# Performance work log

Measured on AMD Instinct MI355X. Metric: run time of the kernel, lower is better.

The kernel has to match this reference:

```python
import jax, jax.numpy as jnp
import numpy as np

NUM_GRAPHS = 5 * 0 + 64  # number of graphs in the batch
NUM_CLASSES = 5


def gcn_conv(x, src, dst, W, b, n_nodes):
    """PyG GCNConv: x' = D^{-1/2} (A+I) D^{-1/2} x W + b (self-loops already in src/dst)."""
    h = x @ W  # [N, out]
    deg = jax.ops.segment_sum(jnp.ones(dst.shape, h.dtype), dst, num_segments=n_nodes)
    dinv = deg ** -0.5  # deg >= 1 thanks to self-loops
    norm = dinv[src] * dinv[dst]  # [E+N]
    msg = h[src] * norm[:, None]  # gather + normalize
    out = jax.ops.segment_sum(msg, dst, num_segments=n_nodes)  # scatter-add
    return out + b


def setup_inputs() -> dict:
    key = jax.random.key(0)
    ks = jax.random.split(key, 12)
    N, E, D_IN, D_H, D_F = 50000, 500000, 128, 256, 256
    x = jax.random.normal(ks[0], (N, D_IN), dtype=jnp.float32)
    edge_index = jax.random.randint(ks[1], (2, E), 0, N, dtype=jnp.int64)
    batch = jnp.sort(jax.random.randint(ks[2], (N,), 0, NUM_GRAPHS, dtype=jnp.int64))
    def lin(k, fi, fo):
        s = 1.0 / np.sqrt(fi)
        return jax.random.uniform(k, (fi, fo), jnp.float32, -s, s)
    return {
        "x": x, "edge_index": edge_index, "batch": batch,
        "W0": lin(ks[3], D_IN, D_H), "b0": jnp.zeros((D_H,), jnp.float32),
        "W1": lin(ks[4], D_H, D_H),  "b1": jnp.zeros((D_H,), jnp.float32),
        "W2": lin(ks[5], D_H, D_H),  "b2": jnp.zeros((D_H,), jnp.float32),
        "Wc1": lin(ks[6], D_H, D_F), "bc1": jnp.zeros((D_F,), jnp.float32),
        "Wc2": lin(ks[7], D_F, NUM_CLASSES), "bc2": jnp.zeros((NUM_CLASSES,), jnp.float32),
    }


def reference(x, edge_index, batch, W0, b0, W1, b1, W2, b2, Wc1, bc1, Wc2, bc2):
    n_nodes = x.shape[0]
    loops = jnp.arange(n_nodes, dtype=edge_index.dtype)
    src = jnp.concatenate([edge_index[0], loops])
    dst = jnp.concatenate([edge_index[1], loops])

    h = jax.nn.relu(gcn_conv(x, src, dst, W0, b0, n_nodes))
    h = jax.nn.relu(gcn_conv(h, src, dst, W1, b1, n_nodes))
    h = jax.nn.relu(gcn_conv(h, src, dst, W2, b2, n_nodes))

    # global_mean_pool over batch ids
    sums = jax.ops.segment_sum(h, batch, num_segments=NUM_GRAPHS)
    cnts = jax.ops.segment_sum(jnp.ones((n_nodes,), h.dtype), batch, num_segments=NUM_GRAPHS)
    g = sums / jnp.maximum(cnts, 1.0)[:, None]  # [NUM_GRAPHS, D_H]

    # classifier MLP (dropout inactive at eval)
    out = jax.nn.relu(g @ Wc1 + bc1) @ Wc2 + bc2
    return out
```

## Files before the change

### kernel.cpp

```cpp
#include <hip/hip_runtime.h>
#include <hip/hip_fp16.h>

typedef short s16x8 __attribute__((ext_vector_type(8)));
typedef float fx4 __attribute__((ext_vector_type(4)));

#define AS_G(p) ((const __attribute__((address_space(1))) void*)(p))
#define AS_L(p) ((__attribute__((address_space(3))) void*)(p))

struct __align__(8) half4 { __half2 lo, hi; };

__device__ inline unsigned short f32_to_bf16(float f) {
    unsigned int u = __float_as_uint(f);
    return (unsigned short)((u + 0x7fffu + ((u >> 16) & 1u)) >> 16);
}
__device__ inline float bf16_to_f32(unsigned short b) {
    return __uint_as_float(((unsigned int)b) << 16);
}
__device__ inline void split2(float a, unsigned short& hi, unsigned short& lo) {
    hi = f32_to_bf16(a);
    lo = f32_to_bf16(a - bf16_to_f32(hi));
}


__global__ void k_degx(const int* __restrict__ dst, int E, int* __restrict__ deg, int degB,
                       const float* __restrict__ x, __half* __restrict__ xh, int nx) {
    if (blockIdx.x < (unsigned)degB) {
        int i = blockIdx.x * 256 + threadIdx.x;
        if (i < E) atomicAdd(&deg[dst[i]], 1);
    } else {
        int i = (blockIdx.x - degB) * 1024 + threadIdx.x * 4;
        if (i < nx) {
            float4 v = *(const float4*)&x[i];
            __half2 h0(__float2half(v.x), __float2half(v.y));
            __half2 h1(__float2half(v.z), __float2half(v.w));
            *(__half2*)&xh[i] = h0;
            *(__half2*)&xh[i + 2] = h1;
        }
    }
}

__global__ void k_scan1w(const int* __restrict__ deg, int N, int nb,
                         int* __restrict__ part, int* __restrict__ bsum, float* __restrict__ dinv,
                         const float* __restrict__ W0, unsigned short* __restrict__ h0, unsigned short* __restrict__ l0,
                         const float* __restrict__ W1, unsigned short* __restrict__ h1, unsigned short* __restrict__ l1,
                         const float* __restrict__ W2, unsigned short* __restrict__ h2, unsigned short* __restrict__ l2,
                         int DIN, int DH) {
    __shared__ int s[256];
    if (blockIdx.x < (unsigned)nb) {
        int i = blockIdx.x * 256 + threadIdx.x;
        int v = (i < N) ? deg[i] : 0;
        if (i < N) dinv[i] = 1.0f / sqrtf((float)(v + 1));
        s[threadIdx.x] = v;
        __syncthreads();
        for (int off = 1; off < 256; off <<= 1) {
            int t = (threadIdx.x >= off) ? s[threadIdx.x - off] : 0;
            __syncthreads();
            s[threadIdx.x] += t;
            __syncthreads();
        }
        if (i < N) part[i] = s[threadIdx.x] - v;
        if (threadIdx.x == 255) bsum[blockIdx.x] = s[255];
    } else {
        int i = (blockIdx.x - nb) * 256 + threadIdx.x;
        const int n0 = DIN * DH, n1 = DH * DH;
        const float* W; unsigned short *hT, *lT; int K, li;
        if (i < n0) { W = W0; hT = h0; lT = l0; K = DIN; li = i; }
        else if (i < n0 + n1) { W = W1; hT = h1; lT = l1; K = DH; li = i - n0; }
        else if (i < n0 + 2 * n1) { W = W2; hT = h2; lT = l2; K = DH; li = i - n0 - n1; }
        else return;
        int k = li / DH, n = li - k * DH;
        unsigned short h, l;
        split2(W[li], h, l);
        hT[(size_t)n * K + k] = h;
        lT[(size_t)n * K + k] = l;
    }
}

__global__ void k_scan2(int* __restrict__ bsum, int nb,
                        const int* __restrict__ batch, int N, int ngraphs, int* __restrict__ gstart) {
    int g = threadIdx.x;
    if (g <= ngraphs) {
        if (g == ngraphs) gstart[g] = N;
        else {
            int lo = 0, hi = N;
            while (lo < hi) {
                int mid = (lo + hi) >> 1;
                if (batch[mid] < g) lo = mid + 1; else hi = mid;
            }
            gstart[g] = lo;
        }
    }
    __shared__ int s[256];
    int v = (threadIdx.x < nb) ? bsum[threadIdx.x] : 0;
    s[threadIdx.x] = v;
    __syncthreads();
    for (int off = 1; off < 256; off <<= 1) {
        int t = (threadIdx.x >= off) ? s[threadIdx.x - off] : 0;
        __syncthreads();
        s[threadIdx.x] += t;
        __syncthreads();
    }
    if (threadIdx.x < nb) bsum[threadIdx.x] = s[threadIdx.x] - v;
}

__global__ void k_scan3(const int* __restrict__ part, const int* __restrict__ bsum, int N, int E,
                        int* __restrict__ rowptr, int* __restrict__ cursor) {
    int i = blockIdx.x * 256 + threadIdx.x;
    if (i < N) {
        int v = part[i] + bsum[blockIdx.x];
        rowptr[i] = v;
        cursor[i] = v;
    }
    if (i == 0) rowptr[N] = E;
}

__global__ void k_fill(const int* __restrict__ src, const int* __restrict__ dst, int E,
                       const float* __restrict__ dinv, int* __restrict__ cursor,
                       int* __restrict__ col, float* __restrict__ nrm) {
    int e = blockIdx.x * blockDim.x + threadIdx.x;
    if (e < E) {
        int s = src[e], d = dst[e];
        int p = atomicAdd(&cursor[d], 1);
        col[p] = s;
        nrm[p] = dinv[s] * dinv[d];
    }
}


__global__ __launch_bounds__(256) void k_gemm_mfma(
    const unsigned short* __restrict__ Ahi, const unsigned short* __restrict__ Alo,
    const unsigned short* __restrict__ BhiT, const unsigned short* __restrict__ BloT,
    const float* __restrict__ bias, __half* __restrict__ C, int Nrows, int K) {
    __shared__ __align__(16) unsigned short sAhi[128 * 32];
    __shared__ __align__(16) unsigned short sAlo[128 * 32];
    __shared__ __align__(16) unsigned short sBhi[128 * 32];
    __shared__ __align__(16) unsigned short sBlo[128 * 32];

    const int tid = threadIdx.x;
    const int wid = tid >> 6, lane = tid & 63;
    const int row0 = blockIdx.y * 128;
    const int col0 = blockIdx.x * 128;
    const int wrow = wid & 1, wcol = wid >> 1;
    const int quad = lane >> 4, l16 = lane & 15;

    const unsigned short* garr = (wid == 0) ? Ahi : (wid == 1) ? Alo : (wid == 2) ? BhiT : BloT;
    unsigned short* sarr = (wid == 0) ? sAhi : (wid == 1) ? sAlo : (wid == 2) ? sBhi : sBlo;
    const bool isA = (wid < 2);

    const unsigned short* gp[8];
#pragma unroll
    for (int i = 0; i < 8; ++i) {
        int r = 16 * i + (lane >> 2);
        int s = lane & 3;
        int q = (s - (r >> 1)) & 3;
        int grow = isA ? min(row0 + r, Nrows - 1) : (col0 + r);
        gp[i] = garr + (size_t)grow * K + q * 8;
    }

    int aidx[4], bidx[4];
#pragma unroll
    for (int t = 0; t < 4; ++t) {
        int ra = wrow * 64 + t * 16 + l16;
        aidx[t] = ra * 32 + ((quad + (ra >> 1)) & 3) * 8;
        int rb = wcol * 64 + t * 16 + l16;
        bidx[t] = rb * 32 + ((quad + (rb >> 1)) & 3) * 8;
    }

    fx4 acc[4][4] = {};

    for (int k0 = 0; k0 < K; k0 += 32) {
#pragma unroll
        for (int i = 0; i < 8; ++i)
            __builtin_amdgcn_global_load_lds(AS_G(gp[i] + k0), AS_L((char*)sarr + i * 1024), 16, 0, 0);
        __syncthreads();

        s16x8 ah[4], al[4];
#pragma unroll
        for (int mi = 0; mi < 4; ++mi) {
            ah[mi] = *(const s16x8*)&sAhi[aidx[mi]];
            al[mi] = *(const s16x8*)&sAlo[aidx[mi]];
        }
#pragma unroll
        for (int nj = 0; nj < 4; ++nj) {
            s16x8 bh = *(const s16x8*)&sBhi[bidx[nj]];
            s16x8 bl = *(const s16x8*)&sBlo[bidx[nj]];
#pragma unroll
            for (int mi = 0; mi < 4; ++mi) {
                acc[mi][nj] = __builtin_amdgcn_mfma_f32_16x16x32_bf16(ah[mi], bh, acc[mi][nj], 0, 0, 0);
                acc[mi][nj] = __builtin_amdgcn_mfma_f32_16x16x32_bf16(ah[mi], bl, acc[mi][nj], 0, 0, 0);
                acc[mi][nj] = __builtin_amdgcn_mfma_f32_16x16x32_bf16(al[mi], bh, acc[mi][nj], 0, 0, 0);
            }
        }
        __syncthreads();
    }

#pragma unroll
    for (int mi = 0; mi < 4; ++mi) {
        const int rbase = row0 + wrow * 64 + mi * 16 + quad * 4;
#pragma unroll
        for (int nj = 0; nj < 4; ++nj) {
            const int c = col0 + wcol * 64 + nj * 16 + l16;
            const float bc = bias[c];
#pragma unroll
            for (int reg = 0; reg < 4; ++reg) {
                int r = rbase + reg;
                if (r < Nrows) C[(size_t)r * 256 + c] = __float2half(fmaxf(acc[mi][nj][reg] + bc, 0.f));
            }
        }
    }
}

__global__ __launch_bounds__(256) void k_gemm_pool(
    const unsigned short* __restrict__ Ahi, const unsigned short* __restrict__ Alo,
    const unsigned short* __restrict__ BhiT, const unsigned short* __restrict__ BloT,
    const float* __restrict__ bias, const int* __restrict__ batch,
    float* __restrict__ gsum, int Nrows, int K) {
    __shared__ __align__(16) unsigned short sAhi[128 * 32];
    __shared__ __align__(16) unsigned short sAlo[128 * 32];
    __shared__ __align__(16) unsigned short sBhi[128 * 32];
    __shared__ __align__(16) unsigned short sBlo[128 * 32];

    const int tid = threadIdx.x;
    const int wid = tid >> 6, lane = tid & 63;
    const int row0 = blockIdx.y * 128;
    const int col0 = blockIdx.x * 128;
    const int wrow = wid & 1, wcol = wid >> 1;
    const int quad = lane >> 4, l16 = lane & 15;

    const unsigned short* garr = (wid == 0) ? Ahi : (wid == 1) ? Alo : (wid == 2) ? BhiT : BloT;
    unsigned short* sarr = (wid == 0) ? sAhi : (wid == 1) ? sAlo : (wid == 2) ? sBhi : sBlo;
    const bool isA = (wid < 2);

    const unsigned short* gp[8];
#pragma unroll
    for (int i = 0; i < 8; ++i) {
        int r = 16 * i + (lane >> 2);
        int s = lane & 3;
        int q = (s - (r >> 1)) & 3;
        int grow = isA ? min(row0 + r, Nrows - 1) : (col0 + r);
        gp[i] = garr + (size_t)grow * K + q * 8;
    }

    int aidx[4], bidx[4];
#pragma unroll
    for (int t = 0; t < 4; ++t) {
        int ra = wrow * 64 + t * 16 + l16;
        aidx[t] = ra * 32 + ((quad + (ra >> 1)) & 3) * 8;
        int rb = wcol * 64 + t * 16 + l16;
        bidx[t] = rb * 32 + ((quad + (rb >> 1)) & 3) * 8;
    }

    fx4 acc[4][4] = {};

    for (int k0 = 0; k0 < K; k0 += 32) {
#pragma unroll
        for (int i = 0; i < 8; ++i)
            __builtin_amdgcn_global_load_lds(AS_G(gp[i] + k0), AS_L((char*)sarr + i * 1024), 16, 0, 0);
        __syncthreads();

        s16x8 ah[4], al[4];
#pragma unroll
        for (int mi = 0; mi < 4; ++mi) {
            ah[mi] = *(const s16x8*)&sAhi[aidx[mi]];
            al[mi] = *(const s16x8*)&sAlo[aidx[mi]];
        }
#pragma unroll
        for (int nj = 0; nj < 4; ++nj) {
            s16x8 bh = *(const s16x8*)&sBhi[bidx[nj]];
            s16x8 bl = *(const s16x8*)&sBlo[bidx[nj]];
#pragma unroll
            for (int mi = 0; mi < 4; ++mi) {
                acc[mi][nj] = __builtin_amdgcn_mfma_f32_16x16x32_bf16(ah[mi], bh, acc[mi][nj], 0, 0, 0);
                acc[mi][nj] = __builtin_amdgcn_mfma_f32_16x16x32_bf16(ah[mi], bl, acc[mi][nj], 0, 0, 0);
                acc[mi][nj] = __builtin_amdgcn_mfma_f32_16x16x32_bf16(al[mi], bh, acc[mi][nj], 0, 0, 0);
            }
        }
        __syncthreads();
    }

    int bg[4][4];
#pragma unroll
    for (int mi = 0; mi < 4; ++mi)
#pragma unroll
        for (int reg = 0; reg < 4; ++reg) {
            int r = row0 + wrow * 64 + mi * 16 + quad * 4 + reg;
            bg[mi][reg] = (r < Nrows) ? batch[r] : -1;
        }
    const int gfirst = batch[row0 < Nrows ? row0 : (Nrows - 1)];
    const int glast  = batch[min(row0 + 127, Nrows - 1)];

#pragma unroll
    for (int nj = 0; nj < 4; ++nj) {
        const int c = col0 + wcol * 64 + nj * 16 + l16;
        const float bc = bias[c];
        for (int g = gfirst; g <= glast; ++g) {
            float s = 0.f;
#pragma unroll
            for (int mi = 0; mi < 4; ++mi)
#pragma unroll
                for (int reg = 0; reg < 4; ++reg)
                    if (bg[mi][reg] == g) s += fmaxf(acc[mi][nj][reg] + bc, 0.f);
            s += __shfl_xor(s, 16);
            s += __shfl_xor(s, 32);
            if (quad == 0) atomicAdd(&gsum[g * 256 + c], s);
        }
    }
}


__global__ __launch_bounds__(256) void k_agg256(const __half* __restrict__ H, const int* __restrict__ rowptr,
                                                const int* __restrict__ col, const float* __restrict__ nrm,
                                                const float* __restrict__ dinv,
                                                unsigned short* __restrict__ outHi,
                                                unsigned short* __restrict__ outLo, int N) {
    const int wave = threadIdx.x >> 6, lane = threadIdx.x & 63;
    const int v = blockIdx.x * 4 + wave;
    if (v >= N) return;

    const float di = dinv[v];
    const float selfn = di * di;
    half4 hv = ((const half4*)&H[(size_t)v * 256])[lane];
    float2 s0 = __half22float2(hv.lo), s1 = __half22float2(hv.hi);
    float ax = selfn * s0.x, ay = selfn * s0.y, az = selfn * s1.x, aw = selfn * s1.y;

    int e = rowptr[v];
    const int end = rowptr[v + 1];
    for (; e + 8 <= end; e += 8) {
        int u[8]; float w[8]; half4 g[8];
#pragma unroll
        for (int j = 0; j < 8; ++j) { u[j] = col[e + j]; w[j] = nrm[e + j]; }
#pragma unroll
        for (int j = 0; j < 8; ++j) g[j] = ((const half4*)&H[(size_t)u[j] * 256])[lane];
#pragma unroll
        for (int j = 0; j < 8; ++j) {
            float2 f0 = __half22float2(g[j].lo), f1 = __half22float2(g[j].hi);
            ax += w[j] * f0.x; ay += w[j] * f0.y; az += w[j] * f1.x; aw += w[j] * f1.y;
        }
    }
    for (; e < end; ++e) {
        const int u = col[e];
        const float w = nrm[e];
        half4 g = ((const half4*)&H[(size_t)u * 256])[lane];
        float2 f0 = __half22float2(g.lo), f1 = __half22float2(g.hi);
        ax += w * f0.x; ay += w * f0.y; az += w * f1.x; aw += w * f1.y;
    }

    ushort4 hi4, lo4;
    split2(ax, hi4.x, lo4.x);
    split2(ay, hi4.y, lo4.y);
    split2(az, hi4.z, lo4.z);
    split2(aw, hi4.w, lo4.w);
    ((ushort4*)outHi)[(size_t)v * 64 + lane] = hi4;
    ((ushort4*)outLo)[(size_t)v * 64 + lane] = lo4;
}

__global__ __launch_bounds__(256) void k_agg128(const __half* __restrict__ X, const int* __restrict__ rowptr,
                                                const int* __restrict__ col, const float* __restrict__ nrm,
                                                const float* __restrict__ dinv,
                                                unsigned short* __restrict__ outHi,
                                                unsigned short* __restrict__ outLo, int N) {
    const int half = threadIdx.x >> 5, sub = threadIdx.x & 31;
    const int v = blockIdx.x * 8 + half;
    if (v >= N) return;

    const float di = dinv[v];
    const float selfn = di * di;
    half4 hv = ((const half4*)&X[(size_t)v * 128])[sub];
    float2 s0 = __half22float2(hv.lo), s1 = __half22float2(hv.hi);
    float ax = selfn * s0.x, ay = selfn * s0.y, az = selfn * s1.x, aw = selfn * s1.y;

    int e = rowptr[v];
    const int end = rowptr[v + 1];
    for (; e + 4 <= end; e += 4) {
        int u[4]; float w[4]; half4 g[4];
#pragma unroll
        for (int j = 0; j < 4; ++j) { u[j] = col[e + j]; w[j] = nrm[e + j]; }
#pragma unroll
        for (int j = 0; j < 4; ++j) g[j] = ((const half4*)&X[(size_t)u[j] * 128])[sub];
#pragma unroll
        for (int j = 0; j < 4; ++j) {
            float2 f0 = __half22float2(g[j].lo), f1 = __half22float2(g[j].hi);
            ax += w[j] * f0.x; ay += w[j] * f0.y; az += w[j] * f1.x; aw += w[j] * f1.y;
        }
    }
    for (; e < end; ++e) {
        const int u = col[e];
        const float w = nrm[e];
        half4 g = ((const half4*)&X[(size_t)u * 128])[sub];
        float2 f0 = __half22float2(g.lo), f1 = __half22float2(g.hi);
        ax += w * f0.x; ay += w * f0.y; az += w * f1.x; aw += w * f1.y;
    }

    ushort4 hi4, lo4;
    split2(ax, hi4.x, lo4.x);
    split2(ay, hi4.y, lo4.y);
    split2(az, hi4.z, lo4.z);
    split2(aw, hi4.w, lo4.w);
    ((ushort4*)outHi)[(size_t)v * 32 + sub] = hi4;
    ((ushort4*)outLo)[(size_t)v * 32 + sub] = lo4;
}


__global__ __launch_bounds__(256) void k_poolcls(const float* __restrict__ gsum, const int* __restrict__ gstart,
                                                 const float* __restrict__ Wc1, const float* __restrict__ bc1,
                                                 const float* __restrict__ Wc2, const float* __restrict__ bc2,
                                                 float* __restrict__ out) {
    __shared__ float sg[256], sh[256];
    const int b = blockIdx.x, t = threadIdx.x;
    const float c = (float)(gstart[b + 1] - gstart[b]);
    sg[t] = gsum[b * 256 + t] / fmaxf(c, 1.0f);
    __syncthreads();
    float acc = bc1[t];
    for (int k = 0; k < 256; ++k) acc += sg[k] * Wc1[k * 256 + t];
    sh[t] = fmaxf(acc, 0.f);
    __syncthreads();
    if (t < 5) {
        float o = bc2[t];
        for (int k = 0; k < 256; ++k) o += sh[k] * Wc2[k * 5 + t];
        out[b * 5 + t] = o;
    }
}


extern "C" void kernel_launch(void* const* d_in, const int* in_sizes, int n_in,
                              void* d_out, int out_size, void* d_ws, size_t ws_size,
                              hipStream_t stream) {
    const float* x    = (const float*)d_in[0];
    const int*   eidx = (const int*)d_in[1];
    const int*   batch= (const int*)d_in[2];
    const float* W0 = (const float*)d_in[3];  const float* b0 = (const float*)d_in[4];
    const float* W1 = (const float*)d_in[5];  const float* b1 = (const float*)d_in[6];
    const float* W2 = (const float*)d_in[7];  const float* b2 = (const float*)d_in[8];
    const float* Wc1= (const float*)d_in[9];  const float* bc1= (const float*)d_in[10];
    const float* Wc2= (const float*)d_in[11]; const float* bc2= (const float*)d_in[12];
    float* out = (float*)d_out;

    const int N   = in_sizes[2];
    const int E   = in_sizes[1] / 2;
    const int DIN = in_sizes[0] / N;
    const int DH  = in_sizes[4];
    const int* src = eidx;
    const int* dst = eidx + E;

    char* p = (char*)d_ws;
    auto alloc = [&](size_t bytes) {
        char* r = p;
        p += (bytes + 255) & ~(size_t)255;
        return (void*)r;
    };
    __half*         hbuf = (__half*)alloc((size_t)N * DH * 2);
    __half*         xh   = (__half*)alloc((size_t)N * DIN * 2);
    unsigned short* hhi  = (unsigned short*)alloc((size_t)N * DH * 2);
    unsigned short* hlo  = (unsigned short*)alloc((size_t)N * DH * 2);
    unsigned short* w0hi = (unsigned short*)alloc((size_t)DH * DIN * 2);
    unsigned short* w0lo = (unsigned short*)alloc((size_t)DH * DIN * 2);
    unsigned short* w1hi = (unsigned short*)alloc((size_t)DH * DH * 2);
    unsigned short* w1lo = (unsigned short*)alloc((size_t)DH * DH * 2);
    unsigned short* w2hi = (unsigned short*)alloc((size_t)DH * DH * 2);
    unsigned short* w2lo = (unsigned short*)alloc((size_t)DH * DH * 2);
    int*   deg   = (int*)alloc((size_t)N * 4);
    float* gsum  = (float*)alloc(64 * (size_t)DH * 4);
    float* dinv  = (float*)alloc((size_t)N * 4);
    int*   part  = (int*)alloc((size_t)N * 4);
    int*   bsum  = (int*)alloc(256 * 4);
    int*   rowptr= (int*)alloc((size_t)(N + 1) * 4);
    int*   cursor= (int*)alloc((size_t)N * 4);
    int*   col   = (int*)alloc((size_t)E * 4);
    float* nrm   = (float*)alloc((size_t)E * 4);
    int*   gstart= (int*)alloc(65 * 4);

    hipMemsetAsync(deg, 0, (size_t)((char*)gsum - (char*)deg) + 64 * (size_t)DH * 4, stream);

    const int nb = (N + 255) / 256;
    const int wtot = DIN * DH + 2 * DH * DH;
    const int wb = (wtot + 255) / 256;
    const int degB = (E + 255) / 256;
    const int nx = N * DIN;
    const int xb = (nx + 1023) / 1024;

    k_degx  <<<degB + xb, 256, 0, stream>>>(dst, E, deg, degB, x, xh, nx);
    k_scan1w<<<nb + wb, 256, 0, stream>>>(deg, N, nb, part, bsum, dinv,
                                          W0, w0hi, w0lo, W1, w1hi, w1lo, W2, w2hi, w2lo, DIN, DH);
    k_scan2 <<<1, 256, 0, stream>>>(bsum, nb, batch, N, 64, gstart);
    k_scan3 <<<nb, 256, 0, stream>>>(part, bsum, N, E, rowptr, cursor);
    k_fill  <<<(E + 255) / 256, 256, 0, stream>>>(src, dst, E, dinv, cursor, col, nrm);

    dim3 gemmGrid(DH / 128, (N + 127) / 128);

    k_agg128<<<(N + 7) / 8, 256, 0, stream>>>(xh, rowptr, col, nrm, dinv, hhi, hlo, N);
    k_gemm_mfma<<<gemmGrid, 256, 0, stream>>>(hhi, hlo, w0hi, w0lo, b0, hbuf, N, DIN);
    k_agg256<<<(N + 3) / 4, 256, 0, stream>>>(hbuf, rowptr, col, nrm, dinv, hhi, hlo, N);
    k_gemm_mfma<<<gemmGrid, 256, 0, stream>>>(hhi, hlo, w1hi, w1lo, b1, hbuf, N, DH);
    k_agg256<<<(N + 3) / 4, 256, 0, stream>>>(hbuf, rowptr, col, nrm, dinv, hhi, hlo, N);
    k_gemm_pool<<<gemmGrid, 256, 0, stream>>>(hhi, hlo, w2hi, w2lo, b2, batch, gsum, N, DH);

    k_poolcls<<<64, 256, 0, stream>>>(gsum, gstart, Wc1, bc1, Wc2, bc2, out);
}
```

Before: 397.3 us.

## Double-buffer GEMM LDS tiles and fold scan2 into scan3 and poolcls

Both MFMA GEMM kernels now use two LDS buffers, issuing global-to-LDS loads for the next K chunk before computing the current one, with one barrier per iteration instead of two. The single-block k_scan2 launch is removed: each scan3 block reduces the preceding block sums itself, and the graph-boundary binary search moves into k_poolcls. This cuts a serialized launch and overlaps memory loads with MFMA work. In exchange LDS use doubles to 64KB per block, which may lower occupancy, and the async LDS writes into the other buffer may need a wait before the barrier to be correct.

```diff
diff --git a/kernel.cpp b/kernel.cpp
--- a/kernel.cpp
+++ b/kernel.cpp
@@ -76,38 +76,20 @@
     }
 }
 
-__global__ void k_scan2(int* __restrict__ bsum, int nb,
-                        const int* __restrict__ batch, int N, int ngraphs, int* __restrict__ gstart) {
-    int g = threadIdx.x;
-    if (g <= ngraphs) {
-        if (g == ngraphs) gstart[g] = N;
-        else {
-            int lo = 0, hi = N;
-            while (lo < hi) {
-                int mid = (lo + hi) >> 1;
-                if (batch[mid] < g) lo = mid + 1; else hi = mid;
-            }
-            gstart[g] = lo;
-        }
-    }
+__global__ void k_scan3(const int* __restrict__ part, const int* __restrict__ bsum, int nb,
+                        int N, int E, int* __restrict__ rowptr, int* __restrict__ cursor) {
     __shared__ int s[256];
-    int v = (threadIdx.x < nb) ? bsum[threadIdx.x] : 0;
-    s[threadIdx.x] = v;
+    const int t = threadIdx.x;
+    s[t] = (t < nb && t < (int)blockIdx.x) ? bsum[t] : 0;
     __syncthreads();
-    for (int off = 1; off < 256; off <<= 1) {
-        int t = (threadIdx.x >= off) ? s[threadIdx.x - off] : 0;
+    for (int off = 128; off > 0; off >>= 1) {
+        if (t < off) s[t] += s[t + off];
         __syncthreads();
-        s[threadIdx.x] += t;
-        __syncthreads();
-    }
-    if (threadIdx.x < nb) bsum[threadIdx.x] = s[threadIdx.x] - v;
-}
-
-__global__ void k_scan3(const int* __restrict__ part, const int* __restrict__ bsum, int N, int E,
-                        int* __restrict__ rowptr, int* __restrict__ cursor) {
-    int i = blockIdx.x * 256 + threadIdx.x;
+    }
+    const int base = s[0];
+    int i = blockIdx.x * 256 + t;
     if (i < N) {
-        int v = part[i] + bsum[blockIdx.x];
+        int v = part[i] + base;
         rowptr[i] = v;
         cursor[i] = v;
     }
@@ -131,10 +113,7 @@
     const unsigned short* __restrict__ Ahi, const unsigned short* __restrict__ Alo,
     const unsigned short* __restrict__ BhiT, const unsigned short* __restrict__ BloT,
     const float* __restrict__ bias, __half* __restrict__ C, int Nrows, int K) {
-    __shared__ __align__(16) unsigned short sAhi[128 * 32];
-    __shared__ __align__(16) unsigned short sAlo[128 * 32];
-    __shared__ __align__(16) unsigned short sBhi[128 * 32];
-    __shared__ __align__(16) unsigned short sBlo[128 * 32];
+    __shared__ __align__(16) unsigned short smem[2][4][128 * 32];
 
     const int tid = threadIdx.x;
     const int wid = tid >> 6, lane = tid & 63;
@@ -144,7 +123,6 @@
     const int quad = lane >> 4, l16 = lane & 15;
 
     const unsigned short* garr = (wid == 0) ? Ahi : (wid == 1) ? Alo : (wid == 2) ? BhiT : BloT;
-    unsigned short* sarr = (wid == 0) ? sAhi : (wid == 1) ? sAlo : (wid == 2) ? sBhi : sBlo;
     const bool isA = (wid < 2);
 
     const unsigned short* gp[8];
@@ -167,12 +145,26 @@
     }
 
     fx4 acc[4][4] = {};
-
-    for (int k0 = 0; k0 < K; k0 += 32) {
-#pragma unroll
-        for (int i = 0; i < 8; ++i)
-            __builtin_amdgcn_global_load_lds(AS_G(gp[i] + k0), AS_L((char*)sarr + i * 1024), 16, 0, 0);
-        __syncthreads();
+    const int nch = K / 32;
+
+#pragma unroll
+    for (int i = 0; i < 8; ++i)
+        __builtin_amdgcn_global_load_lds(AS_G(gp[i]), AS_L((char*)smem[0][wid] + i * 1024), 16, 0, 0);
+    __syncthreads();
+
+    for (int t = 0; t < nch; ++t) {
+        const int buf = t & 1;
+        if (t + 1 < nch) {
+#pragma unroll
+            for (int i = 0; i < 8; ++i)
+                __builtin_amdgcn_global_load_lds(AS_G(gp[i] + (t + 1) * 32),
+                                                 AS_L((char*)smem[1 - buf][wid] + i * 1024), 16, 0, 0);
+        }
+
+        const unsigned short* sAhi = smem[buf][0];
+        const unsigned short* sAlo = smem[buf][1];
+        const unsigned short* sBhi = smem[buf][2];
+        const unsigned short* sBlo = smem[buf][3];
 
         s16x8 ah[4], al[4];
 #pragma unroll
@@ -191,7 +183,7 @@
                 acc[mi][nj] = __builtin_amdgcn_mfma_f32_16x16x32_bf16(al[mi], bh, acc[mi][nj], 0, 0, 0);
             }
         }
-        __syncthreads();
+        if (t + 1 < nch) __syncthreads();
     }
 
 #pragma unroll
@@ -215,10 +207,7 @@
     const unsigned short* __restrict__ BhiT, const unsigned short* __restrict__ BloT,
     const float* __restrict__ bias, const int* __restrict__ batch,
     float* __restrict__ gsum, int Nrows, int K) {
-    __shared__ __align__(16) unsigned short sAhi[128 * 32];
-    __shared__ __align__(16) unsigned short sAlo[128 * 32];
-    __shared__ __align__(16) unsigned short sBhi[128 * 32];
-    __shared__ __align__(16) unsigned short sBlo[128 * 32];
+    __shared__ __align__(16) unsigned short smem[2][4][128 * 32];
 
     const int tid = threadIdx.x;
     const int wid = tid >> 6, lane = tid & 63;
@@ -228,7 +217,6 @@
     const int quad = lane >> 4, l16 = lane & 15;
 
     const unsigned short* garr = (wid == 0) ? Ahi : (wid == 1) ? Alo : (wid == 2) ? BhiT : BloT;
-    unsigned short* sarr = (wid == 0) ? sAhi : (wid == 1) ? sAlo : (wid == 2) ? sBhi : sBlo;
     const bool isA = (wid < 2);
 
     const unsigned short* gp[8];
@@ -251,12 +239,26 @@
     }
 
     fx4 acc[4][4] = {};
-
-    for (int k0 = 0; k0 < K; k0 += 32) {
-#pragma unroll
-        for (int i = 0; i < 8; ++i)
-            __builtin_amdgcn_global_load_lds(AS_G(gp[i] + k0), AS_L((char*)sarr + i * 1024), 16, 0, 0);
-        __syncthreads();
+    const int nch = K / 32;
+
+#pragma unroll
+    for (int i = 0; i < 8; ++i)
+        __builtin_amdgcn_global_load_lds(AS_G(gp[i]), AS_L((char*)smem[0][wid] + i * 1024), 16, 0, 0);
+    __syncthreads();
+
+    for (int t = 0; t < nch; ++t) {
+        const int buf = t & 1;
+        if (t + 1 < nch) {
+#pragma unroll
+            for (int i = 0; i < 8; ++i)
+                __builtin_amdgcn_global_load_lds(AS_G(gp[i] + (t + 1) * 32),
+                                                 AS_L((char*)smem[1 - buf][wid] + i * 1024), 16, 0, 0);
+        }
+
+        const unsigned short* sAhi = smem[buf][0];
+        const unsigned short* sAlo = smem[buf][1];
+        const unsigned short* sBhi = smem[buf][2];
+        const unsigned short* sBlo = smem[buf][3];
 
         s16x8 ah[4], al[4];
 #pragma unroll
@@ -275,7 +277,7 @@
                 acc[mi][nj] = __builtin_amdgcn_mfma_f32_16x16x32_bf16(al[mi], bh, acc[mi][nj], 0, 0, 0);
             }
         }
-        __syncthreads();
+        if (t + 1 < nch) __syncthreads();
     }
 
     int bg[4][4];
@@ -401,13 +403,25 @@
 }
 
 
-__global__ __launch_bounds__(256) void k_poolcls(const float* __restrict__ gsum, const int* __restrict__ gstart,
+__global__ __launch_bounds__(256) void k_poolcls(const float* __restrict__ gsum, const int* __restrict__ batch,
+                                                 int N,
                                                  const float* __restrict__ Wc1, const float* __restrict__ bc1,
                                                  const float* __restrict__ Wc2, const float* __restrict__ bc2,
                                                  float* __restrict__ out) {
     __shared__ float sg[256], sh[256];
+    __shared__ int bounds[2];
     const int b = blockIdx.x, t = threadIdx.x;
-    const float c = (float)(gstart[b + 1] - gstart[b]);
+    if (t < 2) {
+        int target = b + t;
+        int lo = 0, hi = N;
+        while (lo < hi) {
+            int mid = (lo + hi) >> 1;
+            if (batch[mid] < target) lo = mid + 1; else hi = mid;
+        }
+        bounds[t] = lo;
+    }
+    __syncthreads();
+    const float c = (float)(bounds[1] - bounds[0]);
     sg[t] = gsum[b * 256 + t] / fmaxf(c, 1.0f);
     __syncthreads();
     float acc = bc1[t];
@@ -467,7 +481,6 @@
     int*   cursor= (int*)alloc((size_t)N * 4);
     int*   col   = (int*)alloc((size_t)E * 4);
     float* nrm   = (float*)alloc((size_t)E * 4);
-    int*   gstart= (int*)alloc(65 * 4);
 
     hipMemsetAsync(deg, 0, (size_t)((char*)gsum - (char*)deg) + 64 * (size_t)DH * 4, stream);
 
@@ -481,8 +494,7 @@
     k_degx  <<<degB + xb, 256, 0, stream>>>(dst, E, deg, degB, x, xh, nx);
     k_scan1w<<<nb + wb, 256, 0, stream>>>(deg, N, nb, part, bsum, dinv,
                                           W0, w0hi, w0lo, W1, w1hi, w1lo, W2, w2hi, w2lo, DIN, DH);
-    k_scan2 <<<1, 256, 0, stream>>>(bsum, nb, batch, N, 64, gstart);
-    k_scan3 <<<nb, 256, 0, stream>>>(part, bsum, N, E, rowptr, cursor);
+    k_scan3 <<<nb, 256, 0, stream>>>(part, bsum, nb, N, E, rowptr, cursor);
     k_fill  <<<(E + 255) / 256, 256, 0, stream>>>(src, dst, E, dinv, cursor, col, nrm);
 
     dim3 gemmGrid(DH / 128, (N + 127) / 128);
@@ -494,5 +506,5 @@
     k_agg256<<<(N + 3) / 4, 256, 0, stream>>>(hbuf, rowptr, col, nrm, dinv, hhi, hlo, N);
     k_gemm_pool<<<gemmGrid, 256, 0, stream>>>(hhi, hlo, w2hi, w2lo, b2, batch, gsum, N, DH);
 
-    k_poolcls<<<64, 256, 0, stream>>>(gsum, gstart, Wc1, bc1, Wc2, bc2, out);
-}
+    k_poolcls<<<64, 256, 0, stream>>>(gsum, batch, N, Wc1, bc1, Wc2, bc2, out);
+}
```

Result: no change. 398.6 us (+0.3%).
